# Kernel optimization log

Hardware: AMD Instinct MI355X
Metric: run time of the kernel (lower is better)

## Reference

```python
import jax, jax.numpy as jnp
import numpy as np

CROP_H, CROP_W = 14, 14
EXTRAPOLATION_VALUE = 0.0


def setup_inputs() -> dict:
    key = jax.random.key(0)
    k1, k2, k3 = jax.random.split(key, 3)
    image = jax.random.normal(k1, (8, 256, 200, 200), dtype=jnp.float32)
    boxes = jax.random.uniform(k2, (1000, 4), dtype=jnp.float32)  # (y1, x1, y2, x2) normalized
    box_indices = jax.random.randint(k3, (1000,), 0, 8, dtype=jnp.int32)
    return {"image": image, "boxes": boxes, "box_indices": box_indices}


def _gather_corners(image, box_indices, y_idx, x_idx):
    # image: [N, C, H, W]; y_idx: [B, ch]; x_idx: [B, cw] -> [B, C, ch, cw]
    g = image[box_indices[:, None, None], :, y_idx[:, :, None], x_idx[:, None, :]]  # [B, ch, cw, C]
    return jnp.transpose(g, (0, 3, 1, 2))


def _crop_and_resize(image, boxes, box_indices):
    N, C, H, W = image.shape
    y1, x1, y2, x2 = boxes[:, 0], boxes[:, 1], boxes[:, 2], boxes[:, 3]  # [B]

    h_scale = (y2 - y1) * (H - 1) / (CROP_H - 1)  # [B]
    w_scale = (x2 - x1) * (W - 1) / (CROP_W - 1)

    t_y = jnp.arange(CROP_H, dtype=boxes.dtype)
    t_x = jnp.arange(CROP_W, dtype=boxes.dtype)
    in_y = y1[:, None] * (H - 1) + t_y[None, :] * h_scale[:, None]  # [B, ch]
    in_x = x1[:, None] * (W - 1) + t_x[None, :] * w_scale[:, None]  # [B, cw]

    # extrapolation masks (True = out of range)
    mask_y = (in_y > H - 1) | (in_y < 0)  # [B, ch]
    mask_x = (in_x > W - 1) | (in_x < 0)  # [B, cw]
    valid = ~(mask_y[:, :, None] | mask_x[:, None, :])  # [B, ch, cw]
    in_y = jnp.where(mask_y, 0.0, in_y)
    in_x = jnp.where(mask_x, 0.0, in_x)

    top_y = jnp.floor(in_y).astype(jnp.int32)   # [B, ch]
    bot_y = jnp.ceil(in_y).astype(jnp.int32)
    left_x = jnp.floor(in_x).astype(jnp.int32)  # [B, cw]
    right_x = jnp.ceil(in_x).astype(jnp.int32)
    y_lerp = in_y - top_y.astype(in_y.dtype)    # [B, ch]
    x_lerp = in_x - left_x.astype(in_x.dtype)   # [B, cw]

    tl = _gather_corners(image, box_indices, top_y, left_x)   # [B, C, ch, cw]
    tr = _gather_corners(image, box_indices, top_y, right_x)
    bl = _gather_corners(image, box_indices, bot_y, left_x)
    br = _gather_corners(image, box_indices, bot_y, right_x)

    xl = x_lerp[:, None, None, :]  # broadcast over C, ch
    top = tl + xl * (tr - tl)
    bottom = bl + xl * (br - bl)
    crop = top + y_lerp[:, None, :, None] * (bottom - top)  # [B, C, ch, cw]

    m = valid.astype(image.dtype)[:, None, :, :]  # [B, 1, ch, cw]
    return crop * m + (1.0 - m) * EXTRAPOLATION_VALUE


def reference(image, boxes, box_indices):
    return _crop_and_resize(image, boxes, box_indices)
```

## Files before the change

### kernel.cpp

```cpp
#include <hip/hip_runtime.h>

#define CROP_H 14
#define CROP_W 14
#define IMG_H 200
#define IMG_W 200
#define IMG_C 256
#define N_IMG 8
#define N_BOXES 1000
#define ELEMS_PER_BOX (IMG_C * CROP_H * CROP_W)
#define BLOCKS_PER_BOX (ELEMS_PER_BOX / 256)

__global__ __launch_bounds__(512) void bin_boxes_kernel(
    const int* __restrict__ box_idx, int* __restrict__ order)
{
    __shared__ int counts[N_IMG];
    __shared__ int offsets[N_IMG];
    int tid  = threadIdx.x;
    int wave = tid >> 6;
    int lane = tid & 63;

    int cnt = 0;
    for (int i = lane; i < N_BOXES; i += 64) cnt += (box_idx[i] == wave) ? 1 : 0;
    for (int off = 32; off; off >>= 1) cnt += __shfl_down(cnt, off);
    if (lane == 0) counts[wave] = cnt;
    __syncthreads();
    if (tid == 0) {
        int s = 0;
        for (int i = 0; i < N_IMG; i++) { offsets[i] = s; s += counts[i]; }
    }
    __syncthreads();

    int base = offsets[wave];
    for (int i0 = 0; i0 < N_BOXES; i0 += 64) {
        int i = i0 + lane;
        bool p = (i < N_BOXES) && (box_idx[i] == wave);
        unsigned long long m = __ballot(p);
        unsigned long long below = m & ((1ull << lane) - 1ull);
        if (p) order[base + __popcll(below)] = i;
        base += __popcll(m);
    }
}

__global__ __launch_bounds__(256) void crop_resize_kernel(
    const float* __restrict__ image,
    const float* __restrict__ boxes,
    const int*   __restrict__ box_idx,
    const int*   __restrict__ order,
    float*       __restrict__ out)
{
    int pos    = blockIdx.x / BLOCKS_PER_BOX;
    int within = blockIdx.x % BLOCKS_PER_BOX;
    int b      = order[pos];
    int elem   = within * 256 + threadIdx.x;

    int x = elem % CROP_W;
    int t = elem / CROP_W;
    int y = t % CROP_H;
    int c = t / CROP_H;

    float y1 = boxes[b * 4 + 0];
    float x1 = boxes[b * 4 + 1];
    float y2 = boxes[b * 4 + 2];
    float x2 = boxes[b * 4 + 3];

    float h_scale = (y2 - y1) * (float)(IMG_H - 1) / (float)(CROP_H - 1);
    float w_scale = (x2 - x1) * (float)(IMG_W - 1) / (float)(CROP_W - 1);

    float in_y = y1 * (float)(IMG_H - 1) + (float)y * h_scale;
    float in_x = x1 * (float)(IMG_W - 1) + (float)x * w_scale;

    size_t oidx = ((size_t)b * IMG_C + c) * (CROP_H * CROP_W) + y * CROP_W + x;

    bool bad = (in_y > (float)(IMG_H - 1)) || (in_y < 0.0f) ||
               (in_x > (float)(IMG_W - 1)) || (in_x < 0.0f);
    if (bad) { out[oidx] = 0.0f; return; }

    int ty = (int)floorf(in_y);
    int by = (int)ceilf(in_y);
    int lx = (int)floorf(in_x);
    int rx = (int)ceilf(in_x);
    float yl = in_y - (float)ty;
    float xl = in_x - (float)lx;

    int n = box_idx[b];
    const float* __restrict__ plane =
        image + ((size_t)n * IMG_C + c) * (size_t)(IMG_H * IMG_W);

    float tl = plane[ty * IMG_W + lx];
    float tr = plane[ty * IMG_W + rx];
    float bl = plane[by * IMG_W + lx];
    float br = plane[by * IMG_W + rx];

    float top = tl + xl * (tr - tl);
    float bot = bl + xl * (br - bl);
    out[oidx] = top + yl * (bot - top);
}

extern "C" void kernel_launch(void* const* d_in, const int* in_sizes, int n_in,
                              void* d_out, int out_size, void* d_ws, size_t ws_size,
                              hipStream_t stream) {
    const float* image   = (const float*)d_in[0];
    const float* boxes   = (const float*)d_in[1];
    const int*   box_idx = (const int*)d_in[2];
    float* out  = (float*)d_out;
    int* order  = (int*)d_ws;

    bin_boxes_kernel<<<1, 512, 0, stream>>>(box_idx, order);

    int grid = N_BOXES * BLOCKS_PER_BOX;
    crop_resize_kernel<<<grid, 256, 0, stream>>>(image, boxes, box_idx, order, out);
}
```

Before: 284.0 us.

## Stage box sample rows into shared memory with float4 loads per channel chunk

```diff
diff --git a/kernel.cpp b/kernel.cpp
--- a/kernel.cpp
+++ b/kernel.cpp
@@ -7,8 +7,11 @@
 #define IMG_C 256
 #define N_IMG 8
 #define N_BOXES 1000
-#define ELEMS_PER_BOX (IMG_C * CROP_H * CROP_W)
-#define BLOCKS_PER_BOX (ELEMS_PER_BOX / 256)
+#define PLANE (IMG_H * IMG_W)
+#define CPB 16
+#define CHUNKS (IMG_C / CPB)
+#define NSLOT (2 * CROP_H)
+#define BUF_STRIDE 212
 
 __global__ __launch_bounds__(512) void bin_boxes_kernel(
     const int* __restrict__ box_idx, int* __restrict__ order)
@@ -48,15 +51,22 @@
     const int*   __restrict__ order,
     float*       __restrict__ out)
 {
-    int pos    = blockIdx.x / BLOCKS_PER_BOX;
-    int within = blockIdx.x % BLOCKS_PER_BOX;
-    int b      = order[pos];
-    int elem   = within * 256 + threadIdx.x;
+    __shared__ int   s_slotrow[NSLOT];
+    __shared__ float s_yl[CROP_H];
+    __shared__ int   s_ymask[CROP_H];
+    __shared__ int   s_lx[CROP_W], s_rx[CROP_W];
+    __shared__ float s_xl[CROP_W];
+    __shared__ int   s_xmask[CROP_W];
+    __shared__ int   s_xmin4, s_rowlen4, s_safe;
+    __shared__ float s_rcp;
+    __shared__ __align__(16) float buf[NSLOT][BUF_STRIDE];
 
-    int x = elem % CROP_W;
-    int t = elem / CROP_W;
-    int y = t % CROP_H;
-    int c = t / CROP_H;
+    int tid   = threadIdx.x;
+    int pos   = blockIdx.x / CHUNKS;
+    int chunk = blockIdx.x % CHUNKS;
+    int b     = order[pos];
+    int n     = box_idx[b];
+    int c0    = chunk * CPB;
 
     float y1 = boxes[b * 4 + 0];
     float x1 = boxes[b * 4 + 1];
@@ -66,34 +76,97 @@
     float h_scale = (y2 - y1) * (float)(IMG_H - 1) / (float)(CROP_H - 1);
     float w_scale = (x2 - x1) * (float)(IMG_W - 1) / (float)(CROP_W - 1);
 
-    float in_y = y1 * (float)(IMG_H - 1) + (float)y * h_scale;
-    float in_x = x1 * (float)(IMG_W - 1) + (float)x * w_scale;
+    if (tid < CROP_H) {
+        float in_y = y1 * (float)(IMG_H - 1) + (float)tid * h_scale;
+        int m = (in_y > (float)(IMG_H - 1)) || (in_y < 0.0f);
+        if (m) in_y = 0.0f;
+        int ty = (int)floorf(in_y);
+        int by = (int)ceilf(in_y);
+        s_slotrow[2 * tid]     = ty;
+        s_slotrow[2 * tid + 1] = by;
+        s_yl[tid]    = in_y - (float)ty;
+        s_ymask[tid] = m;
+    }
+    if (tid >= 16 && tid < 16 + CROP_W) {
+        int x = tid - 16;
+        float in_x = x1 * (float)(IMG_W - 1) + (float)x * w_scale;
+        int m = (in_x > (float)(IMG_W - 1)) || (in_x < 0.0f);
+        if (m) in_x = 0.0f;
+        int lx = (int)floorf(in_x);
+        int rx = (int)ceilf(in_x);
+        s_lx[x] = lx;
+        s_rx[x] = rx;
+        s_xl[x] = in_x - (float)lx;
+        s_xmask[x] = m;
+    }
+    __syncthreads();
+    if (tid == 0) {
+        int xmin = IMG_W, xmax = 0;
+        for (int x = 0; x < CROP_W; x++) {
+            xmin = min(xmin, s_lx[x]);
+            xmax = max(xmax, s_rx[x]);
+        }
+        int xmin4 = xmin & ~3;
+        int nf    = xmax - xmin4 + 1;
+        int rl4   = (nf + 3) >> 2;
+        s_xmin4   = xmin4;
+        s_rowlen4 = rl4;
+        s_rcp     = 1.0f / (float)rl4;
+        s_safe    = (xmin4 + rl4 * 4 <= IMG_W);
+    }
+    __syncthreads();
 
-    size_t oidx = ((size_t)b * IMG_C + c) * (CROP_H * CROP_W) + y * CROP_W + x;
+    int   xmin4   = s_xmin4;
+    int   rowlen4 = s_rowlen4;
+    int   safe    = s_safe;
+    float rcp     = s_rcp;
+    int   total4  = NSLOT * rowlen4;
 
-    bool bad = (in_y > (float)(IMG_H - 1)) || (in_y < 0.0f) ||
-               (in_x > (float)(IMG_W - 1)) || (in_x < 0.0f);
-    if (bad) { out[oidx] = 0.0f; return; }
+    size_t plane_base = ((size_t)n * IMG_C + c0) * (size_t)PLANE;
+    size_t out_base   = ((size_t)b * IMG_C + c0) * (size_t)(CROP_H * CROP_W);
 
-    int ty = (int)floorf(in_y);
-    int by = (int)ceilf(in_y);
-    int lx = (int)floorf(in_x);
-    int rx = (int)ceilf(in_x);
-    float yl = in_y - (float)ty;
-    float xl = in_x - (float)lx;
+    for (int cc = 0; cc < CPB; ++cc) {
+        const float* __restrict__ plane = image + plane_base + (size_t)cc * PLANE;
 
-    int n = box_idx[b];
-    const float* __restrict__ plane =
-        image + ((size_t)n * IMG_C + c) * (size_t)(IMG_H * IMG_W);
+        for (int i = tid; i < total4; i += 256) {
+            int r   = (int)(((float)i + 0.5f) * rcp);
+            int off = i - r * rowlen4;
+            int row = s_slotrow[r];
+            const float* src = plane + row * IMG_W + xmin4 + off * 4;
+            float4 v;
+            if (safe || off != rowlen4 - 1) {
+                v = *(const float4*)src;
+            } else {
+                int base = xmin4 + off * 4;
+                const float* prow = plane + row * IMG_W;
+                v.x = prow[min(base + 0, IMG_W - 1)];
+                v.y = prow[min(base + 1, IMG_W - 1)];
+                v.z = prow[min(base + 2, IMG_W - 1)];
+                v.w = prow[min(base + 3, IMG_W - 1)];
+            }
+            *(float4*)&buf[r][off * 4] = v;
+        }
+        __syncthreads();
 
-    float tl = plane[ty * IMG_W + lx];
-    float tr = plane[ty * IMG_W + rx];
-    float bl = plane[by * IMG_W + lx];
-    float br = plane[by * IMG_W + rx];
-
-    float top = tl + xl * (tr - tl);
-    float bot = bl + xl * (br - bl);
-    out[oidx] = top + yl * (bot - top);
+        if (tid < CROP_H * CROP_W) {
+            int y = tid / CROP_W;
+            int x = tid % CROP_W;
+            int kl = s_lx[x] - xmin4;
+            int kr = s_rx[x] - xmin4;
+            float xl = s_xl[x];
+            float yl = s_yl[y];
+            float tl = buf[2 * y][kl];
+            float tr = buf[2 * y][kr];
+            float bl = buf[2 * y + 1][kl];
+            float br = buf[2 * y + 1][kr];
+            float top = tl + xl * (tr - tl);
+            float bot = bl + xl * (br - bl);
+            float v = top + yl * (bot - top);
+            if (s_ymask[y] | s_xmask[x]) v = 0.0f;
+            out[out_base + (size_t)cc * (CROP_H * CROP_W) + tid] = v;
+        }
+        __syncthreads();
+    }
 }
 
 extern "C" void kernel_launch(void* const* d_in, const int* in_sizes, int n_in,
@@ -107,6 +180,6 @@
 
     bin_boxes_kernel<<<1, 512, 0, stream>>>(box_idx, order);
 
-    int grid = N_BOXES * BLOCKS_PER_BOX;
+    int grid = N_BOXES * CHUNKS;
     crop_resize_kernel<<<grid, 256, 0, stream>>>(image, boxes, box_idx, order, out);
 }
```

Result: slower. 492.3 us (+73.3%).
